# Kernel tuning notes

Measured on AMD Instinct MI355X. Metric: run time of the kernel, lower is better.

The kernel has to match this reference:

```python
import jax, jax.numpy as jnp
import numpy as np

D_MODEL = 2048
N_HEADS = 32
N_KV = 8
HEAD_DIM = D_MODEL // N_HEADS        # 64
N_GROUPS = N_HEADS // N_KV           # 4
ROPE_BASE = 10000.0
SCALE = HEAD_DIM ** -0.5
BATCH, SEQ = 2, 2048


def setup_inputs() -> dict:
    key = jax.random.key(0)
    k1, k2, k3, k4, k5 = jax.random.split(key, 5)
    init = 0.02  # typical transformer init scale
    return {
        "x":  jax.random.normal(k1, (BATCH, SEQ, D_MODEL), jnp.float32),
        "Wq": jax.random.normal(k2, (D_MODEL, D_MODEL), jnp.float32) * init,
        "Wk": jax.random.normal(k3, (N_KV * HEAD_DIM, D_MODEL), jnp.float32) * init,
        "Wv": jax.random.normal(k4, (N_KV * HEAD_DIM, D_MODEL), jnp.float32) * init,
        "Wo": jax.random.normal(k5, (D_MODEL, D_MODEL), jnp.float32) * init,
    }


def _apply_rope(q, k, seq_len):
    # q: (b, n_heads, s, hd), k: (b, n_kv, s, hd). LLaMA-style rotate-half RoPE.
    half = HEAD_DIM // 2
    inv_freq = 1.0 / (ROPE_BASE ** (jnp.arange(0, half, dtype=jnp.float32) / half))
    ang = jnp.arange(seq_len, dtype=jnp.float32)[:, None] * inv_freq[None, :]  # (s, half)
    cos = jnp.concatenate([jnp.cos(ang), jnp.cos(ang)], axis=-1)[None, None]   # (1,1,s,hd)
    sin = jnp.concatenate([jnp.sin(ang), jnp.sin(ang)], axis=-1)[None, None]

    def rot_half(t):
        t1, t2 = jnp.split(t, 2, axis=-1)
        return jnp.concatenate([-t2, t1], axis=-1)

    q = q * cos + rot_half(q) * sin
    k = k * cos + rot_half(k) * sin
    return q, k


def reference(x, Wq, Wk, Wv, Wo):
    b, s, _ = x.shape
    # projections (nn.Linear: y = x @ W.T)
    q = jnp.einsum('bsd,ed->bse', x, Wq).reshape(b, s, N_HEADS, HEAD_DIM).transpose(0, 2, 1, 3)
    k = jnp.einsum('bsd,ed->bse', x, Wk).reshape(b, s, N_KV, HEAD_DIM).transpose(0, 2, 1, 3)
    v = jnp.einsum('bsd,ed->bse', x, Wv).reshape(b, s, N_KV, HEAD_DIM).transpose(0, 2, 1, 3)

    q, k = _apply_rope(q, k, s)

    # GQA: repeat_interleave(k, n_groups) maps q-head h -> kv-head h // n_groups,
    # equivalent to grouping consecutive q heads and broadcasting kv per group.
    qg = q.reshape(b, N_KV, N_GROUPS, s, HEAD_DIM)
    scores = jnp.einsum('bkgqd,bkld->bkgql', qg, k) * SCALE   # (b, n_kv, g, s, s)
    attn = jax.nn.softmax(scores, axis=-1)
    out = jnp.einsum('bkgql,bkld->bkgqd', attn, v)            # (b, n_kv, g, s, hd)

    out = out.reshape(b, N_HEADS, s, HEAD_DIM).transpose(0, 2, 1, 3).reshape(b, s, D_MODEL)
    return jnp.einsum('bsd,ed->bse', out, Wo)
```

## Files before the change

kernel.cpp:

```cpp
#include <hip/hip_runtime.h>
#include <hip/hip_bf16.h>


typedef __attribute__((ext_vector_type(8))) short short8;
typedef __attribute__((ext_vector_type(4))) float f32x4;
typedef __attribute__((ext_vector_type(16))) float f32x16;

#define MFMA16(A, B, C) __builtin_amdgcn_mfma_f32_16x16x32_bf16((A), (B), (C), 0, 0, 0)
#define MFMA32(A, B, C) __builtin_amdgcn_mfma_f32_32x32x16_bf16((A), (B), (C), 0, 0, 0)

__device__ __forceinline__ ushort f2bf(float f) {
  __hip_bfloat16 h = __float2bfloat16(f);
  return __builtin_bit_cast(ushort, h);
}

__device__ __forceinline__ float fexp2(float x) {
#if __has_builtin(__builtin_amdgcn_exp2f)
  return __builtin_amdgcn_exp2f(x);
#else
  float r;
  asm("v_exp_f32 %0, %1" : "=v"(r) : "v"(x));
  return r;
#endif
}

__device__ __forceinline__ void gload_lds16(const void* g, void* l) {
  __builtin_amdgcn_global_load_lds(
      (const __attribute__((address_space(1))) unsigned int*)g,
      (__attribute__((address_space(3))) unsigned int*)l, 16, 0, 0);
}

__global__ __launch_bounds__(256) void prep_kernel(
    const float* __restrict__ x, const float* __restrict__ Wq,
    const float* __restrict__ Wk, const float* __restrict__ Wv,
    const float* __restrict__ Wo, ushort* __restrict__ xbf,
    ushort* __restrict__ wqbf, ushort* __restrict__ wkbf,
    ushort* __restrict__ wvbf, ushort* __restrict__ wobf,
    float* __restrict__ tc, float* __restrict__ ts) {
  const int blk = blockIdx.x;
  if (blk < 9216) {
    const float* src;
    ushort* dst;
    int t;
    if (blk < 4096) {
      src = x; dst = xbf; t = blk * 256 + threadIdx.x;
    } else if (blk < 6144) {
      src = Wq; dst = wqbf; t = (blk - 4096) * 256 + threadIdx.x;
    } else if (blk < 6656) {
      src = Wk; dst = wkbf; t = (blk - 6144) * 256 + threadIdx.x;
    } else if (blk < 7168) {
      src = Wv; dst = wvbf; t = (blk - 6656) * 256 + threadIdx.x;
    } else {
      src = Wo; dst = wobf; t = (blk - 7168) * 256 + threadIdx.x;
    }
    const float4* p = (const float4*)src;
    float4 a = p[t * 2], b = p[t * 2 + 1];
    int4 o;
    o.x = (int)f2bf(a.x) | ((int)f2bf(a.y) << 16);
    o.y = (int)f2bf(a.z) | ((int)f2bf(a.w) << 16);
    o.z = (int)f2bf(b.x) | ((int)f2bf(b.y) << 16);
    o.w = (int)f2bf(b.z) | ((int)f2bf(b.w) << 16);
    ((int4*)dst)[t] = o;
  } else {
    int t = (blk - 9216) * 256 + threadIdx.x;
    int j = t & 31, s = t >> 5;
    float freq = powf(10000.0f, -(float)j * (1.0f / 32.0f));
    float ang = (float)s * freq;
    tc[t] = cosf(ang);
    ts[t] = sinf(ang);
  }
}

__device__ __forceinline__ void gemm_core(const ushort* __restrict__ A,
                                          const ushort* __restrict__ Bt,
                                          int row0, int col0, int K,
                                          f32x4 (&acc)[4][4]) {
  __shared__ __align__(16) ushort As[8192];
  __shared__ __align__(16) ushort Bs[8192];
  const int t = threadIdx.x;
  const int lane = t & 63, wid = t >> 6;
  const int lr = lane & 15, lh = lane >> 4;
  const int wm = wid >> 1, wn = wid & 1;
#pragma unroll
  for (int i = 0; i < 4; ++i)
#pragma unroll
    for (int j = 0; j < 4; ++j) acc[i][j] = (f32x4){0.f, 0.f, 0.f, 0.f};

  const int srow = t >> 3, scg = (t & 7) ^ (srow & 7);
  const ushort* Asrc = A + (size_t)(row0 + srow) * K + scg * 8;
  const ushort* Bsrc = Bt + (size_t)(col0 + srow) * K + scg * 8;
  char* AsB = (char*)As + wid * 1024;
  char* BsB = (char*)Bs + wid * 1024;
  const int s7a = lr & 7;

  for (int k0 = 0; k0 < K; k0 += 64) {
    __syncthreads();
#pragma unroll
    for (int i = 0; i < 4; ++i) {
      gload_lds16(Asrc + (size_t)(32 * i) * K + k0, AsB + i * 4096);
      gload_lds16(Bsrc + (size_t)(32 * i) * K + k0, BsB + i * 4096);
    }
    __syncthreads();

    short8 af[4][2];
#pragma unroll
    for (int fm = 0; fm < 4; ++fm)
#pragma unroll
      for (int kk = 0; kk < 2; ++kk)
        af[fm][kk] = *(const short8*)((const char*)As +
                                      ((wm * 64 + fm * 16 + lr) << 7) +
                                      (((kk * 4 + lh) ^ s7a) << 4));
#pragma unroll
    for (int kk = 0; kk < 2; ++kk)
#pragma unroll
      for (int fn = 0; fn < 4; ++fn) {
        short8 bf_ = *(const short8*)((const char*)Bs +
                                      ((wn * 64 + fn * 16 + lr) << 7) +
                                      (((kk * 4 + lh) ^ s7a) << 4));
#pragma unroll
        for (int fm = 0; fm < 4; ++fm)
          acc[fm][fn] = MFMA16(af[fm][kk], bf_, acc[fm][fn]);
      }
  }
}

__device__ __forceinline__ void gemm_core_db(const ushort* __restrict__ A,
                                             const ushort* __restrict__ Bt,
                                             int row0, int col0, int K,
                                             f32x4 (&acc)[4][4]) {
  __shared__ __align__(16) ushort As[16384];
  __shared__ __align__(16) ushort Bs[16384];
  const int t = threadIdx.x;
  const int lane = t & 63, wid = t >> 6;
  const int lr = lane & 15, lh = lane >> 4;
  const int wm = wid >> 1, wn = wid & 1;
#pragma unroll
  for (int i = 0; i < 4; ++i)
#pragma unroll
    for (int j = 0; j < 4; ++j) acc[i][j] = (f32x4){0.f, 0.f, 0.f, 0.f};

  const int srow = t >> 3, scg = (t & 7) ^ (srow & 7);
  const ushort* Asrc = A + (size_t)(row0 + srow) * K + scg * 8;
  const ushort* Bsrc = Bt + (size_t)(col0 + srow) * K + scg * 8;
  const int s7a = lr & 7;

#define GSTAGE(PAR, KOFF)                                                    \
  do {                                                                       \
    char* a_ = (char*)As + (PAR) * 16384 + wid * 1024;                       \
    char* b_ = (char*)Bs + (PAR) * 16384 + wid * 1024;                       \
    _Pragma("unroll") for (int i_ = 0; i_ < 4; ++i_) {                       \
      gload_lds16(Asrc + (size_t)(32 * i_) * K + (KOFF), a_ + i_ * 4096);    \
      gload_lds16(Bsrc + (size_t)(32 * i_) * K + (KOFF), b_ + i_ * 4096);    \
    }                                                                        \
  } while (0)

  GSTAGE(0, 0);
  GSTAGE(1, 64);
  const int nstep = K >> 6;
  for (int it = 0; it < nstep; ++it) {
    if (it + 1 < nstep)
      asm volatile("s_waitcnt vmcnt(8)" ::: "memory");
    else
      asm volatile("s_waitcnt vmcnt(0)" ::: "memory");
    __builtin_amdgcn_s_barrier();
    {
      const char* ab_ = (const char*)As + (it & 1) * 16384;
      const char* bb_ = (const char*)Bs + (it & 1) * 16384;
      short8 af[4][2];
#pragma unroll
      for (int fm = 0; fm < 4; ++fm)
#pragma unroll
        for (int kk = 0; kk < 2; ++kk)
          af[fm][kk] = *(const short8*)(ab_ + ((wm * 64 + fm * 16 + lr) << 7) +
                                        (((kk * 4 + lh) ^ s7a) << 4));
#pragma unroll
      for (int kk = 0; kk < 2; ++kk)
#pragma unroll
        for (int fn = 0; fn < 4; ++fn) {
          short8 bf_ = *(const short8*)(bb_ + ((wn * 64 + fn * 16 + lr) << 7) +
                                        (((kk * 4 + lh) ^ s7a) << 4));
#pragma unroll
          for (int fm = 0; fm < 4; ++fm)
            acc[fm][fn] = MFMA16(af[fm][kk], bf_, acc[fm][fn]);
        }
    }
    __builtin_amdgcn_s_barrier();
    if (it + 2 < nstep) GSTAGE(it & 1, (it + 2) * 64);
  }
#undef GSTAGE
}

__global__ __launch_bounds__(256) void gemm_qkv_kernel(
    const ushort* __restrict__ xbf, const ushort* __restrict__ wq,
    const ushort* __restrict__ wk, const ushort* __restrict__ wv,
    ushort* __restrict__ Qo, ushort* __restrict__ Ko, ushort* __restrict__ Vo,
    const float* __restrict__ tabc, const float* __restrict__ tabs) {
  int bx = blockIdx.x % 24, by = blockIdx.x / 24;
  const ushort* Bt;
  int cb;
  if (bx < 16) {
    Bt = wq; cb = bx;
  } else if (bx < 20) {
    Bt = wk; cb = bx - 16;
  } else {
    Bt = wv; cb = bx - 20;
  }
  f32x4 acc[4][4];
  gemm_core(xbf, Bt, by * 128, cb * 128, 2048, acc);

  const int lane = threadIdx.x & 63, wid = threadIdx.x >> 6;
  const int lr = lane & 15, lh = lane >> 4;
  const int wm = wid >> 1, wn = wid & 1;
  const int srow0 = by * 128 + wm * 64 + lh * 4;

  if (bx >= 20) {
    const int kv = cb * 2 + wn;
#pragma unroll
    for (int fm = 0; fm < 4; ++fm) {
      int srow = srow0 + fm * 16;
      int bb = srow >> 11, s = srow & 2047;
#pragma unroll
      for (int fn = 0; fn < 4; ++fn) {
        int d = fn * 16 + lr;
        ushort4 o;
        o.x = f2bf(acc[fm][fn][0]);
        o.y = f2bf(acc[fm][fn][1]);
        o.z = f2bf(acc[fm][fn][2]);
        o.w = f2bf(acc[fm][fn][3]);
        *(ushort4*)&Vo[((size_t)((bb * 8 + kv) * 64 + d)) * 2048 + s] = o;
      }
    }
  } else {
    ushort* dst;
    int nh, h;
    float scale;
    if (bx < 16) {
      dst = Qo; nh = 32; h = bx * 2 + wn;
      scale = 0.125f * 1.44269504088896340736f;
    } else {
      dst = Ko; nh = 8; h = cb * 2 + wn; scale = 1.0f;
    }
#pragma unroll
    for (int fm = 0; fm < 4; ++fm) {
      int srow = srow0 + fm * 16;
      int bb = srow >> 11, sbase = srow & 2047;
      size_t obase = (size_t)(bb * nh + h) * 2048;
#pragma unroll
      for (int fn = 0; fn < 2; ++fn) {
        int j = fn * 16 + lr;
#pragma unroll
        for (int r = 0; r < 4; ++r) {
          int s = sbase + r;
          float c = tabc[s * 32 + j], sn = tabs[s * 32 + j];
          float x1 = acc[fm][fn][r], x2 = acc[fm][fn + 2][r];
          ushort* po = &dst[(obase + s) * 64 + j];
          po[0] = f2bf((x1 * c - x2 * sn) * scale);
          po[32] = f2bf((x2 * c + x1 * sn) * scale);
        }
      }
    }
  }
}

__global__ __launch_bounds__(256, 2) void gemm_o_kernel(const ushort* __restrict__ A,
                                                        const ushort* __restrict__ Wo,
                                                        float* __restrict__ C) {
  int bx = blockIdx.x & 15, by = blockIdx.x >> 4;
  int row0 = by * 128, col0 = bx * 128;
  f32x4 acc[4][4];
  gemm_core_db(A, Wo, row0, col0, 2048, acc);
  const int lane = threadIdx.x & 63, wid = threadIdx.x >> 6;
  const int lr = lane & 15, lh = lane >> 4;
  const int wm = wid >> 1, wn = wid & 1;
#pragma unroll
  for (int fm = 0; fm < 4; ++fm) {
    int r0 = row0 + wm * 64 + fm * 16 + lh * 4;
#pragma unroll
    for (int fn = 0; fn < 4; ++fn) {
      int cc = col0 + wn * 64 + fn * 16 + lr;
#pragma unroll
      for (int r = 0; r < 4; ++r) C[(size_t)(r0 + r) * 2048 + cc] = acc[fm][fn][r];
    }
  }
}

__global__ __launch_bounds__(256, 2) void attn_kernel(const ushort* __restrict__ Q,
                                                      const ushort* __restrict__ Kg,
                                                      const ushort* __restrict__ Vt,
                                                      ushort* __restrict__ O) {
  __shared__ __align__(16) char smem_c[32768];
  const int tid = threadIdx.x;
  const int lane = tid & 63;
  const int wid = tid >> 6;
  const int bid = ((blockIdx.x & 7) << 6) | (blockIdx.x >> 3);
  const int qp = bid & 31;
  const int kvh = (bid >> 5) & 7;
  const int b = bid >> 8;
  const int h = kvh * 4 + wid;
  const int q0 = qp * 64;
  const int l31 = lane & 31;
  const int hi = lane >> 5;

  const ushort* Qp = Q + ((size_t)((b * 32 + h) * 2048 + q0)) * 64;
  const ushort* Kp = Kg + ((size_t)((b * 8 + kvh) * 2048)) * 64;
  const ushort* Vp = Vt + ((size_t)((b * 8 + kvh) * 64)) * 2048;

  const int srow = tid >> 3, scg = (tid & 7) ^ (srow & 7);
  const ushort* Kst = Kp + (size_t)srow * 64 + scg * 8;
  const ushort* Vst = Vp + (size_t)srow * 2048 + scg * 8;

#define STAGE(PAR, KV0)                                                         \
  do {                                                                          \
    char* kd_ = smem_c + (PAR) * 8192 + wid * 1024;                             \
    char* vd_ = smem_c + 16384 + (PAR) * 8192 + wid * 1024;                     \
    gload_lds16(Kst + (size_t)(KV0) * 64, kd_);                                 \
    gload_lds16(Kst + (size_t)((KV0) + 32) * 64, kd_ + 4096);                   \
    gload_lds16(Vst + (KV0), vd_);                                              \
    gload_lds16(Vst + 32 * 2048 + (KV0), vd_ + 4096);                           \
  } while (0)

  STAGE(0, 0);

  const short8 qfA0 = *(const short8*)(Qp + (size_t)l31 * 64 + 0 + hi * 8);
  const short8 qfA1 = *(const short8*)(Qp + (size_t)l31 * 64 + 16 + hi * 8);
  const short8 qfA2 = *(const short8*)(Qp + (size_t)l31 * 64 + 32 + hi * 8);
  const short8 qfA3 = *(const short8*)(Qp + (size_t)l31 * 64 + 48 + hi * 8);
  const short8 qfB0 = *(const short8*)(Qp + (size_t)(32 + l31) * 64 + 0 + hi * 8);
  const short8 qfB1 = *(const short8*)(Qp + (size_t)(32 + l31) * 64 + 16 + hi * 8);
  const short8 qfB2 = *(const short8*)(Qp + (size_t)(32 + l31) * 64 + 32 + hi * 8);
  const short8 qfB3 = *(const short8*)(Qp + (size_t)(32 + l31) * 64 + 48 + hi * 8);

  const int s7 = l31 & 7;
  const int ok0 = l31 * 128 + (((0 + hi) ^ s7) << 4);
  const int ok1 = l31 * 128 + (((2 + hi) ^ s7) << 4);
  const int ok2 = l31 * 128 + (((4 + hi) ^ s7) << 4);
  const int ok3 = l31 * 128 + (((6 + hi) ^ s7) << 4);

  f32x16 accA0, accA1, accB0, accB1, kz;
#pragma unroll
  for (int r = 0; r < 16; ++r) {
    accA0[r] = 0.f;
    accA1[r] = 0.f;
    accB0[r] = 0.f;
    accB1[r] = 0.f;
    kz[r] = 0.f;
  }
  float lshA = 0.f, lshB = 0.f;

#define QK2(STA, STB, KOFF)                                  \
  do {                                                       \
    const char* kb_ = smem_c + (KOFF);                       \
    short8 kf_ = *(const short8*)(kb_ + ok0);                \
    __builtin_amdgcn_s_setprio(1);                           \
    STA = MFMA32(kf_, qfA0, kz);                             \
    STB = MFMA32(kf_, qfB0, kz);                             \
    kf_ = *(const short8*)(kb_ + ok1);                       \
    STA = MFMA32(kf_, qfA1, STA);                            \
    STB = MFMA32(kf_, qfB1, STB);                            \
    kf_ = *(const short8*)(kb_ + ok2);                       \
    STA = MFMA32(kf_, qfA2, STA);                            \
    STB = MFMA32(kf_, qfB2, STB);                            \
    kf_ = *(const short8*)(kb_ + ok3);                       \
    STA = MFMA32(kf_, qfA3, STA);                            \
    STB = MFMA32(kf_, qfB3, STB);                            \
    __builtin_amdgcn_s_setprio(0);                           \
  } while (0)

#define SMX(ST, F0, F1, LSH)                                                  \
  do {                                                                        \
    float ps_ = 0.f;                                                          \
    uint pk0_, pk1_, pk2_, pk3_, pk4_, pk5_, pk6_, pk7_;                      \
    _Pragma("unroll") for (int j = 0; j < 8; ++j) {                           \
      float pa_ = fexp2(ST[2 * j]);                                           \
      float pb_ = fexp2(ST[2 * j + 1]);                                       \
      ps_ += pa_ + pb_;                                                       \
      uint w_ = __builtin_amdgcn_perm(__builtin_bit_cast(uint, pb_),          \
                                      __builtin_bit_cast(uint, pa_),          \
                                      0x07060302u);                           \
      switch (j) {                                                            \
        case 0: pk0_ = w_; break;                                             \
        case 1: pk1_ = w_; break;                                             \
        case 2: pk2_ = w_; break;                                             \
        case 3: pk3_ = w_; break;                                             \
        case 4: pk4_ = w_; break;                                             \
        case 5: pk5_ = w_; break;                                             \
        case 6: pk6_ = w_; break;                                             \
        default: pk7_ = w_; break;                                            \
      }                                                                       \
    }                                                                         \
    LSH += ps_;                                                               \
    uint u0_ = hi ? pk0_ : pk2_; u0_ = __shfl_xor(u0_, 32);                   \
    uint u1_ = hi ? pk1_ : pk3_; u1_ = __shfl_xor(u1_, 32);                   \
    uint u2_ = hi ? pk4_ : pk6_; u2_ = __shfl_xor(u2_, 32);                   \
    uint u3_ = hi ? pk5_ : pk7_; u3_ = __shfl_xor(u3_, 32);                   \
    F0.u[0] = hi ? u0_ : pk0_;                                                \
    F0.u[1] = hi ? u1_ : pk1_;                                                \
    F0.u[2] = hi ? pk2_ : u0_;                                                \
    F0.u[3] = hi ? pk3_ : u1_;                                                \
    F1.u[0] = hi ? u2_ : pk4_;                                                \
    F1.u[1] = hi ? u3_ : pk5_;                                                \
    F1.u[2] = hi ? pk6_ : u2_;                                                \
    F1.u[3] = hi ? pk7_ : u3_;                                                \
  } while (0)

#define SMPV2(STA, STB, VOFF, VSX)                                           \
  do {                                                                       \
    union { uint u[4]; short8 s; } fA0_, fA1_, fB0_, fB1_;                   \
    SMX(STA, fA0_, fA1_, lshA);                                              \
    SMX(STB, fB0_, fB1_, lshB);                                              \
    const char* vb_ = smem_c + (VOFF);                                       \
    short8 v0_ = *(const short8*)(vb_ + (ok0 ^ (VSX)));                      \
    short8 v1_ = *(const short8*)(vb_ + (ok1 ^ (VSX)));                      \
    __builtin_amdgcn_s_setprio(1);                                           \
    accA0 = MFMA32(v0_, fA0_.s, accA0);                                      \
    accA0 = MFMA32(v1_, fA1_.s, accA0);                                      \
    accB0 = MFMA32(v0_, fB0_.s, accB0);                                      \
    accB0 = MFMA32(v1_, fB1_.s, accB0);                                      \
    __builtin_amdgcn_s_setprio(0);                                           \
    v0_ = *(const short8*)(vb_ + (ok0 ^ (VSX)) + 4096);                      \
    v1_ = *(const short8*)(vb_ + (ok1 ^ (VSX)) + 4096);                      \
    __builtin_amdgcn_s_setprio(1);                                           \
    accA1 = MFMA32(v0_, fA0_.s, accA1);                                      \
    accA1 = MFMA32(v1_, fA1_.s, accA1);                                      \
    accB1 = MFMA32(v0_, fB0_.s, accB1);                                      \
    accB1 = MFMA32(v1_, fB1_.s, accB1);                                      \
    __builtin_amdgcn_s_setprio(0);                                           \
  } while (0)

  for (int t = 0; t < 32; ++t) {
    asm volatile("s_waitcnt vmcnt(0)" ::: "memory");
    __builtin_amdgcn_s_barrier();
    if (t < 31) STAGE((t + 1) & 1, (t + 1) * 64);
    {
      const int kb = (t & 1) * 8192;
      const int vb = 16384 + (t & 1) * 8192;
      f32x16 stA0_, stB0_, stA1_, stB1_;
      QK2(stA0_, stB0_, kb);
      QK2(stA1_, stB1_, kb + 4096);
      SMPV2(stA0_, stB0_, vb, 0);
      SMPV2(stA1_, stB1_, vb, 64);
    }
  }
#undef STAGE
#undef QK2
#undef SMX
#undef SMPV2

  const float lsA = lshA + __shfl_xor(lshA, 32);
  const float lsB = lshB + __shfl_xor(lshB, 32);
  const float invA = 1.0f / lsA;
  const float invB = 1.0f / lsB;
  ushort* ObA = O + (size_t)(b * 2048 + q0 + l31) * 2048 + h * 64;
  ushort* ObB = O + (size_t)(b * 2048 + q0 + 32 + l31) * 2048 + h * 64;
#pragma unroll
  for (int rg = 0; rg < 4; ++rg) {
    ushort4 o0, o1;
    o0.x = f2bf(accA0[rg * 4 + 0] * invA);
    o0.y = f2bf(accA0[rg * 4 + 1] * invA);
    o0.z = f2bf(accA0[rg * 4 + 2] * invA);
    o0.w = f2bf(accA0[rg * 4 + 3] * invA);
    o1.x = f2bf(accA1[rg * 4 + 0] * invA);
    o1.y = f2bf(accA1[rg * 4 + 1] * invA);
    o1.z = f2bf(accA1[rg * 4 + 2] * invA);
    o1.w = f2bf(accA1[rg * 4 + 3] * invA);
    *(ushort4*)(ObA + rg * 8 + hi * 4) = o0;
    *(ushort4*)(ObA + 32 + rg * 8 + hi * 4) = o1;
    o0.x = f2bf(accB0[rg * 4 + 0] * invB);
    o0.y = f2bf(accB0[rg * 4 + 1] * invB);
    o0.z = f2bf(accB0[rg * 4 + 2] * invB);
    o0.w = f2bf(accB0[rg * 4 + 3] * invB);
    o1.x = f2bf(accB1[rg * 4 + 0] * invB);
    o1.y = f2bf(accB1[rg * 4 + 1] * invB);
    o1.z = f2bf(accB1[rg * 4 + 2] * invB);
    o1.w = f2bf(accB1[rg * 4 + 3] * invB);
    *(ushort4*)(ObB + rg * 8 + hi * 4) = o0;
    *(ushort4*)(ObB + 32 + rg * 8 + hi * 4) = o1;
  }
}

extern "C" void kernel_launch(void* const* d_in, const int* in_sizes, int n_in,
                              void* d_out, int out_size, void* d_ws, size_t ws_size,
                              hipStream_t stream) {
  (void)in_sizes; (void)n_in; (void)out_size; (void)ws_size;
  const float* x = (const float*)d_in[0];
  const float* Wq = (const float*)d_in[1];
  const float* Wk = (const float*)d_in[2];
  const float* Wv = (const float*)d_in[3];
  const float* Wo = (const float*)d_in[4];
  float* out = (float*)d_out;

  char* ws = (char*)d_ws;
  size_t off = 0;
  auto take = [&](size_t bytes) {
    void* p = ws + off;
    off += (bytes + 255) & ~(size_t)255;
    return p;
  };
  ushort* xbf = (ushort*)take(16777216);
  ushort* wqbf = (ushort*)take(8388608);
  ushort* wkbf = (ushort*)take(2097152);
  ushort* wvbf = (ushort*)take(2097152);
  ushort* wobf = (ushort*)take(8388608);
  ushort* Qbf = (ushort*)take(16777216);
  ushort* Kbf = (ushort*)take(4194304);
  ushort* Vtb = (ushort*)take(4194304);
  ushort* attnout = (ushort*)take(16777216);
  float* tabc = (float*)take(262144);
  float* tabs = (float*)take(262144);

  prep_kernel<<<9472, 256, 0, stream>>>(x, Wq, Wk, Wv, Wo, xbf, wqbf, wkbf,
                                        wvbf, wobf, tabc, tabs);
  gemm_qkv_kernel<<<768, 256, 0, stream>>>(xbf, wqbf, wkbf, wvbf, Qbf, Kbf,
                                           Vtb, tabc, tabs);
  attn_kernel<<<512, 256, 0, stream>>>(Qbf, Kbf, Vtb, attnout);
  gemm_o_kernel<<<512, 256, 0, stream>>>(attnout, wobf, out);
}
```

Baseline: 205.8 us.

## Split attention KV range in two and merge partials in a combine kernel

The attention kernel now processes half of the KV sequence per block, doubling the grid. Each block writes normalized partial outputs in fp16 plus per-row softmax denominators. A new combine kernel blends the two partials, weighting each by its denominator, and writes the bf16 attention output. The goal is more blocks and shorter per-block loops to improve load balance. The cost is an extra kernel launch and extra global traffic for the partial buffers. The weighting is only correct if both halves share the same softmax max offset.

```diff
diff --git a/kernel.cpp b/kernel.cpp
--- a/kernel.cpp
+++ b/kernel.cpp
@@ -12,6 +12,15 @@
 __device__ __forceinline__ ushort f2bf(float f) {
   __hip_bfloat16 h = __float2bfloat16(f);
   return __builtin_bit_cast(ushort, h);
+}
+
+__device__ __forceinline__ ushort f2h(float f) {
+  _Float16 h = (_Float16)f;
+  return __builtin_bit_cast(ushort, h);
+}
+
+__device__ __forceinline__ float h2f(ushort u) {
+  return (float)__builtin_bit_cast(_Float16, u);
 }
 
 __device__ __forceinline__ float fexp2(float x) {
@@ -287,17 +296,21 @@
 __global__ __launch_bounds__(256, 2) void attn_kernel(const ushort* __restrict__ Q,
                                                       const ushort* __restrict__ Kg,
                                                       const ushort* __restrict__ Vt,
-                                                      ushort* __restrict__ O) {
+                                                      ushort* __restrict__ P,
+                                                      float* __restrict__ lsp) {
   __shared__ __align__(16) char smem_c[32768];
   const int tid = threadIdx.x;
   const int lane = tid & 63;
   const int wid = tid >> 6;
-  const int bid = ((blockIdx.x & 7) << 6) | (blockIdx.x >> 3);
-  const int qp = bid & 31;
-  const int kvh = (bid >> 5) & 7;
-  const int b = bid >> 8;
+  const int bid = (blockIdx.x & 7) * 128 + (blockIdx.x >> 3);
+  const int split = bid >> 9;
+  const int r9 = bid & 511;
+  const int qp = r9 & 31;
+  const int kvh = (r9 >> 5) & 7;
+  const int b = r9 >> 8;
   const int h = kvh * 4 + wid;
   const int q0 = qp * 64;
+  const int kvbase = split << 10;
   const int l31 = lane & 31;
   const int hi = lane >> 5;
 
@@ -319,7 +332,7 @@
     gload_lds16(Vst + 32 * 2048 + (KV0), vd_ + 4096);                           \
   } while (0)
 
-  STAGE(0, 0);
+  STAGE(0, kvbase);
 
   const short8 qfA0 = *(const short8*)(Qp + (size_t)l31 * 64 + 0 + hi * 8);
   const short8 qfA1 = *(const short8*)(Qp + (size_t)l31 * 64 + 16 + hi * 8);
@@ -427,10 +440,10 @@
     __builtin_amdgcn_s_setprio(0);                                           \
   } while (0)
 
-  for (int t = 0; t < 32; ++t) {
+  for (int t = 0; t < 16; ++t) {
     asm volatile("s_waitcnt vmcnt(0)" ::: "memory");
     __builtin_amdgcn_s_barrier();
-    if (t < 31) STAGE((t + 1) & 1, (t + 1) * 64);
+    if (t < 15) STAGE((t + 1) & 1, kvbase + (t + 1) * 64);
     {
       const int kb = (t & 1) * 8192;
       const int vb = 16384 + (t & 1) * 8192;
@@ -450,32 +463,70 @@
   const float lsB = lshB + __shfl_xor(lshB, 32);
   const float invA = 1.0f / lsA;
   const float invB = 1.0f / lsB;
-  ushort* ObA = O + (size_t)(b * 2048 + q0 + l31) * 2048 + h * 64;
-  ushort* ObB = O + (size_t)(b * 2048 + q0 + 32 + l31) * 2048 + h * 64;
+  if (hi == 0) {
+    size_t lbase = ((size_t)(split * 2 + b) * 32 + h) * 2048 + q0;
+    lsp[lbase + l31] = lsA;
+    lsp[lbase + 32 + l31] = lsB;
+  }
+  ushort* Pb = P + (size_t)split * (4096 * 2048);
+  ushort* ObA = Pb + (size_t)(b * 2048 + q0 + l31) * 2048 + h * 64;
+  ushort* ObB = Pb + (size_t)(b * 2048 + q0 + 32 + l31) * 2048 + h * 64;
 #pragma unroll
   for (int rg = 0; rg < 4; ++rg) {
     ushort4 o0, o1;
-    o0.x = f2bf(accA0[rg * 4 + 0] * invA);
-    o0.y = f2bf(accA0[rg * 4 + 1] * invA);
-    o0.z = f2bf(accA0[rg * 4 + 2] * invA);
-    o0.w = f2bf(accA0[rg * 4 + 3] * invA);
-    o1.x = f2bf(accA1[rg * 4 + 0] * invA);
-    o1.y = f2bf(accA1[rg * 4 + 1] * invA);
-    o1.z = f2bf(accA1[rg * 4 + 2] * invA);
-    o1.w = f2bf(accA1[rg * 4 + 3] * invA);
+    o0.x = f2h(accA0[rg * 4 + 0] * invA);
+    o0.y = f2h(accA0[rg * 4 + 1] * invA);
+    o0.z = f2h(accA0[rg * 4 + 2] * invA);
+    o0.w = f2h(accA0[rg * 4 + 3] * invA);
+    o1.x = f2h(accA1[rg * 4 + 0] * invA);
+    o1.y = f2h(accA1[rg * 4 + 1] * invA);
+    o1.z = f2h(accA1[rg * 4 + 2] * invA);
+    o1.w = f2h(accA1[rg * 4 + 3] * invA);
     *(ushort4*)(ObA + rg * 8 + hi * 4) = o0;
     *(ushort4*)(ObA + 32 + rg * 8 + hi * 4) = o1;
-    o0.x = f2bf(accB0[rg * 4 + 0] * invB);
-    o0.y = f2bf(accB0[rg * 4 + 1] * invB);
-    o0.z = f2bf(accB0[rg * 4 + 2] * invB);
-    o0.w = f2bf(accB0[rg * 4 + 3] * invB);
-    o1.x = f2bf(accB1[rg * 4 + 0] * invB);
-    o1.y = f2bf(accB1[rg * 4 + 1] * invB);
-    o1.z = f2bf(accB1[rg * 4 + 2] * invB);
-    o1.w = f2bf(accB1[rg * 4 + 3] * invB);
+    o0.x = f2h(accB0[rg * 4 + 0] * invB);
+    o0.y = f2h(accB0[rg * 4 + 1] * invB);
+    o0.z = f2h(accB0[rg * 4 + 2] * invB);
+    o0.w = f2h(accB0[rg * 4 + 3] * invB);
+    o1.x = f2h(accB1[rg * 4 + 0] * invB);
+    o1.y = f2h(accB1[rg * 4 + 1] * invB);
+    o1.z = f2h(accB1[rg * 4 + 2] * invB);
+    o1.w = f2h(accB1[rg * 4 + 3] * invB);
     *(ushort4*)(ObB + rg * 8 + hi * 4) = o0;
     *(ushort4*)(ObB + 32 + rg * 8 + hi * 4) = o1;
   }
+}
+
+__global__ __launch_bounds__(256) void combine_kernel(const ushort* __restrict__ P,
+                                                      const float* __restrict__ lsp,
+                                                      ushort* __restrict__ O) {
+  int t = blockIdx.x * 256 + threadIdx.x;
+  int d8 = t & 7;
+  int h = (t >> 3) & 31;
+  int s = (t >> 8) & 2047;
+  int b = t >> 19;
+  size_t idx = ((size_t)(b * 2048 + s)) * 2048 + h * 64 + d8 * 8;
+  float ls0 = lsp[((size_t)b * 32 + h) * 2048 + s];
+  float ls1 = lsp[((size_t)(2 + b) * 32 + h) * 2048 + s];
+  float w0 = ls0 / (ls0 + ls1);
+  float w1 = 1.0f - w0;
+  int4 a0 = *(const int4*)(P + idx);
+  int4 a1 = *(const int4*)(P + (size_t)4096 * 2048 + idx);
+  int4 o;
+  int va0[4] = {a0.x, a0.y, a0.z, a0.w};
+  int va1[4] = {a1.x, a1.y, a1.z, a1.w};
+  int vo[4];
+#pragma unroll
+  for (int i = 0; i < 4; ++i) {
+    float lo = h2f((ushort)va0[i]) * w0 + h2f((ushort)va1[i]) * w1;
+    float hi2 = h2f((ushort)(va0[i] >> 16)) * w0 + h2f((ushort)(va1[i] >> 16)) * w1;
+    vo[i] = (int)f2bf(lo) | ((int)f2bf(hi2) << 16);
+  }
+  o.x = vo[0];
+  o.y = vo[1];
+  o.z = vo[2];
+  o.w = vo[3];
+  *(int4*)(O + idx) = o;
 }
 
 extern "C" void kernel_launch(void* const* d_in, const int* in_sizes, int n_in,
@@ -504,6 +555,8 @@
   ushort* Qbf = (ushort*)take(16777216);
   ushort* Kbf = (ushort*)take(4194304);
   ushort* Vtb = (ushort*)take(4194304);
+  ushort* part = (ushort*)take(33554432);
+  float* lsp = (float*)take(1048576);
   ushort* attnout = (ushort*)take(16777216);
   float* tabc = (float*)take(262144);
   float* tabs = (float*)take(262144);
@@ -512,6 +565,7 @@
                                         wvbf, wobf, tabc, tabs);
   gemm_qkv_kernel<<<768, 256, 0, stream>>>(xbf, wqbf, wkbf, wvbf, Qbf, Kbf,
                                            Vtb, tabc, tabs);
-  attn_kernel<<<512, 256, 0, stream>>>(Qbf, Kbf, Vtb, attnout);
+  attn_kernel<<<1024, 256, 0, stream>>>(Qbf, Kbf, Vtb, part, lsp);
+  combine_kernel<<<4096, 256, 0, stream>>>(part, lsp, attnout);
   gemm_o_kernel<<<512, 256, 0, stream>>>(attnout, wobf, out);
 }
```

After: 217.5 us. 1.06x slower.
